# Kernel tuning notes

Measured on AMD Instinct MI355X. Metric: run time of the kernel, lower is better.

Reference implementation:

```python
import jax, jax.numpy as jnp
import numpy as np

HOMO_BOOST_THRD = 0.5
HOMO_LOSS_WEIGHT = 100.0
EPS = 1e-8  # F.cosine_similarity default eps

N_NODES = 50000
N_EDGES = 1600000
D_FEAT = 128
N_TARGET = 5000
N_BKD = 500


def setup_inputs() -> dict:
    key = jax.random.key(0)
    k1, k2, k3, k4, k5 = jax.random.split(key, 5)
    edge_index = jax.random.randint(k1, (2, N_EDGES), 0, N_NODES, dtype=jnp.int64 if jax.config.jax_enable_x64 else jnp.int32)
    edge_weights = jax.random.uniform(k2, (N_EDGES,), dtype=jnp.float32)
    x = jax.random.normal(k3, (N_NODES, D_FEAT), dtype=jnp.float32)
    target_nodes = jax.random.randint(k4, (N_TARGET,), 0, N_NODES)
    bkd_nodes = jax.random.randint(k5, (N_BKD,), 0, N_NODES)
    return {"edge_index": edge_index, "edge_weights": edge_weights, "x": x,
            "target_nodes": target_nodes, "bkd_nodes": bkd_nodes}


def reference(edge_index, edge_weights, x, target_nodes, bkd_nodes):
    n = x.shape[0]
    # membership bitmaps replace per-edge python `in set` checks
    is_bkd = jnp.zeros((n,), dtype=bool).at[bkd_nodes].set(True)
    is_tgt = jnp.zeros((n,), dtype=bool).at[target_nodes].set(True)

    u, v = edge_index[0], edge_index[1]
    # dense_to_sparse in the original drops zero-weight edges
    mask = ((is_bkd[u] & is_tgt[v]) | (is_bkd[v] & is_tgt[u])) & (edge_weights != 0)

    xu = x[u]  # [E, d]
    xv = x[v]  # [E, d]
    dot = jnp.sum(xu * xv, axis=-1)
    nu = jnp.maximum(jnp.linalg.norm(xu, axis=-1), EPS)
    nv = jnp.maximum(jnp.linalg.norm(xv, axis=-1), EPS)
    sims = dot / (nu * nv)  # F.cosine_similarity

    per_edge = jnp.maximum(HOMO_BOOST_THRD - sims, 0.0)  # clamp-at-zero branch
    loss = HOMO_LOSS_WEIGHT * jnp.sum(jnp.where(mask, per_edge, 0.0))
    return loss
```

## Files before the change

### kernel.cpp

```cpp
#include <hip/hip_runtime.h>

#define HOMO_BOOST_THRD 0.5f
#define HOMO_LOSS_WEIGHT 100.0f
#define COS_EPS 1e-8f
#define D_FEAT 128
#define EDGE_BLOCK 256
#define EPT 8
#define QMAX (EDGE_BLOCK * EPT)

#define FLAG_WORDS_MAX 4096

__global__ __launch_bounds__(EDGE_BLOCK) void edge_loss_kernel(
        const int* __restrict__ edge_index,
        const float* __restrict__ edge_weights,
        const float* __restrict__ x,
        const int* __restrict__ target_nodes, int n_tgt,
        const int* __restrict__ bkd_nodes, int n_bkd,
        float* __restrict__ partials, int E, int nwords) {
    __shared__ unsigned int sflags[FLAG_WORDS_MAX];
    __shared__ int q_u[QMAX];
    __shared__ int q_v[QMAX];
    __shared__ int qn;
    __shared__ float wsum[EDGE_BLOCK / 64];

    uint4* s4 = reinterpret_cast<uint4*>(sflags);
    const int nwords4 = (nwords + 3) >> 2;
    for (int i = threadIdx.x; i < nwords4; i += EDGE_BLOCK)
        s4[i] = make_uint4(0u, 0u, 0u, 0u);
    if (threadIdx.x == 0) qn = 0;
    __syncthreads();

    const int n_tgt4 = n_tgt >> 2;
    const int4* t4 = reinterpret_cast<const int4*>(target_nodes);
    for (int i = threadIdx.x; i < n_tgt4; i += EDGE_BLOCK) {
        int4 nd = t4[i];
        atomicOr(&sflags[nd.x >> 4], 2u << ((nd.x & 15) * 2));
        atomicOr(&sflags[nd.y >> 4], 2u << ((nd.y & 15) * 2));
        atomicOr(&sflags[nd.z >> 4], 2u << ((nd.z & 15) * 2));
        atomicOr(&sflags[nd.w >> 4], 2u << ((nd.w & 15) * 2));
    }
    for (int i = (n_tgt4 << 2) + threadIdx.x; i < n_tgt; i += EDGE_BLOCK) {
        int node = target_nodes[i];
        atomicOr(&sflags[node >> 4], 2u << ((node & 15) * 2));
    }
    const int n_bkd4 = n_bkd >> 2;
    const int4* b4 = reinterpret_cast<const int4*>(bkd_nodes);
    for (int i = threadIdx.x; i < n_bkd4; i += EDGE_BLOCK) {
        int4 nd = b4[i];
        atomicOr(&sflags[nd.x >> 4], 1u << ((nd.x & 15) * 2));
        atomicOr(&sflags[nd.y >> 4], 1u << ((nd.y & 15) * 2));
        atomicOr(&sflags[nd.z >> 4], 1u << ((nd.z & 15) * 2));
        atomicOr(&sflags[nd.w >> 4], 1u << ((nd.w & 15) * 2));
    }
    for (int i = (n_bkd4 << 2) + threadIdx.x; i < n_bkd; i += EDGE_BLOCK) {
        int node = bkd_nodes[i];
        atomicOr(&sflags[node >> 4], 1u << ((node & 15) * 2));
    }
    __syncthreads();

    const int base = (blockIdx.x * EDGE_BLOCK + threadIdx.x) * EPT;
    const bool full = (blockIdx.x * EDGE_BLOCK * EPT + EDGE_BLOCK * EPT <= E)
                      && ((E & 3) == 0);

    int us[EPT], vs[EPT];
    if (full) {
        const int4* up = reinterpret_cast<const int4*>(edge_index + base);
        const int4* vp = reinterpret_cast<const int4*>(edge_index + E + base);
        #pragma unroll
        for (int qd = 0; qd < EPT / 4; ++qd) {
            int4 uq = up[qd];
            int4 vq = vp[qd];
            us[qd*4+0] = uq.x; us[qd*4+1] = uq.y; us[qd*4+2] = uq.z; us[qd*4+3] = uq.w;
            vs[qd*4+0] = vq.x; vs[qd*4+1] = vq.y; vs[qd*4+2] = vq.z; vs[qd*4+3] = vq.w;
        }
    } else {
        #pragma unroll
        for (int k = 0; k < EPT; ++k) {
            int e = base + k;
            bool ok = (e < E);
            us[k] = ok ? edge_index[e] : 0;
            vs[k] = ok ? edge_index[E + e] : 0;
        }
    }

    #pragma unroll
    for (int k = 0; k < EPT; ++k) {
        bool valid = full || (base + k < E);
        unsigned fu = (sflags[us[k] >> 4] >> ((us[k] & 15) * 2)) & 3u;
        unsigned fv = (sflags[vs[k] >> 4] >> ((vs[k] & 15) * 2)) & 3u;
        bool m = valid && ((((fu & (fv >> 1)) | (fv & (fu >> 1))) & 1u) != 0);
        if (m) {
            float w = edge_weights[base + k];
            if (w != 0.0f) {
                int qi = atomicAdd(&qn, 1);
                q_u[qi] = us[k];
                q_v[qi] = vs[k];
            }
        }
    }
    __syncthreads();

    const int lane = threadIdx.x & 63;
    const int wid  = threadIdx.x >> 6;
    const int nq   = qn;
    float wval = 0.0f;

    for (int i = wid * 2; i < nq; i += 2 * (EDGE_BLOCK / 64)) {
        bool has1 = (i + 1 < nq);
        int u0 = q_u[i], v0 = q_v[i];
        int u1 = has1 ? q_u[i + 1] : u0;
        int v1 = has1 ? q_v[i + 1] : v0;

        float2 a0 = reinterpret_cast<const float2*>(x + (size_t)u0 * D_FEAT)[lane];
        float2 c0 = reinterpret_cast<const float2*>(x + (size_t)v0 * D_FEAT)[lane];
        float2 a1 = reinterpret_cast<const float2*>(x + (size_t)u1 * D_FEAT)[lane];
        float2 c1 = reinterpret_cast<const float2*>(x + (size_t)v1 * D_FEAT)[lane];

        float d0 = a0.x * c0.x + a0.y * c0.y;
        float p0 = a0.x * a0.x + a0.y * a0.y;
        float q0 = c0.x * c0.x + c0.y * c0.y;
        float d1 = a1.x * c1.x + a1.y * c1.y;
        float p1 = a1.x * a1.x + a1.y * a1.y;
        float q1 = c1.x * c1.x + c1.y * c1.y;
        #pragma unroll
        for (int off = 1; off < 64; off <<= 1) {
            d0 += __shfl_xor(d0, off, 64);
            p0 += __shfl_xor(p0, off, 64);
            q0 += __shfl_xor(q0, off, 64);
            d1 += __shfl_xor(d1, off, 64);
            p1 += __shfl_xor(p1, off, 64);
            q1 += __shfl_xor(q1, off, 64);
        }
        if (lane == 0) {
            float nu0 = fmaxf(sqrtf(p0), COS_EPS);
            float nv0 = fmaxf(sqrtf(q0), COS_EPS);
            wval += fmaxf(HOMO_BOOST_THRD - d0 / (nu0 * nv0), 0.0f);
            if (has1) {
                float nu1 = fmaxf(sqrtf(p1), COS_EPS);
                float nv1 = fmaxf(sqrtf(q1), COS_EPS);
                wval += fmaxf(HOMO_BOOST_THRD - d1 / (nu1 * nv1), 0.0f);
            }
        }
    }

    if (lane == 0) wsum[wid] = wval;
    __syncthreads();
    if (threadIdx.x == 0)
        partials[blockIdx.x] = wsum[0] + wsum[1] + wsum[2] + wsum[3];
}

__global__ void reduce_kernel(const float* __restrict__ partials, int n,
                              float* __restrict__ out) {
    __shared__ float wsum[16];
    float s = 0.0f;
    for (int i = threadIdx.x; i < n; i += blockDim.x) s += partials[i];
    #pragma unroll
    for (int off = 32; off > 0; off >>= 1) s += __shfl_down(s, off, 64);
    if ((threadIdx.x & 63) == 0) wsum[threadIdx.x >> 6] = s;
    __syncthreads();
    if (threadIdx.x == 0) {
        float t = 0.0f;
        for (int w = 0; w < (int)(blockDim.x >> 6); ++w) t += wsum[w];
        out[0] = t * HOMO_LOSS_WEIGHT;
    }
}

extern "C" void kernel_launch(void* const* d_in, const int* in_sizes, int n_in,
                              void* d_out, int out_size, void* d_ws, size_t ws_size,
                              hipStream_t stream) {
    const int*   edge_index   = (const int*)  d_in[0];
    const float* edge_weights = (const float*)d_in[1];
    const float* x            = (const float*)d_in[2];
    const int*   target_nodes = (const int*)  d_in[3];
    const int*   bkd_nodes    = (const int*)  d_in[4];

    const int E     = in_sizes[0] / 2;
    const int N     = in_sizes[2] / D_FEAT;
    const int n_tgt = in_sizes[3];
    const int n_bkd = in_sizes[4];

    const int nwords = (N + 15) / 16;
    float* partials = (float*)d_ws;

    const int nblocks = (E + EDGE_BLOCK * EPT - 1) / (EDGE_BLOCK * EPT);
    edge_loss_kernel<<<nblocks, EDGE_BLOCK, 0, stream>>>(
        edge_index, edge_weights, x, target_nodes, n_tgt, bkd_nodes, n_bkd,
        partials, E, nwords);

    reduce_kernel<<<1, 1024, 0, stream>>>(partials, nblocks, (float*)d_out);
}
```

Measured before the change: 13.58 us.

## Build membership bitmap once in a separate kernel and copy into shared memory

Moves construction of the backdoor/target bitmap out of every edge block into a single one-block prekernel that writes it to workspace. Each edge block then copies the prebuilt bitmap into shared memory instead of zeroing it and running about 5500 shared atomics. The block size also doubles to 512, which halves the number of blocks, and the final reduce uses 512 threads. The cost is an extra kernel launch that runs serially before the main kernel, plus a global read of the bitmap in every block.

```diff
diff --git a/kernel.cpp b/kernel.cpp
--- a/kernel.cpp
+++ b/kernel.cpp
@@ -4,63 +4,71 @@
 #define HOMO_LOSS_WEIGHT 100.0f
 #define COS_EPS 1e-8f
 #define D_FEAT 128
-#define EDGE_BLOCK 256
+#define EDGE_BLOCK 512
 #define EPT 8
+#define NWAVES (EDGE_BLOCK / 64)
 #define QMAX (EDGE_BLOCK * EPT)
 
 #define FLAG_WORDS_MAX 4096
+
+__global__ void build_flags_kernel(const int* __restrict__ target_nodes, int n_tgt,
+                                   const int* __restrict__ bkd_nodes, int n_bkd,
+                                   unsigned int* __restrict__ flags_w, int nwords) {
+    uint4* f4 = reinterpret_cast<uint4*>(flags_w);
+    const int nwords4 = (nwords + 3) >> 2;
+    for (int i = threadIdx.x; i < nwords4; i += blockDim.x)
+        f4[i] = make_uint4(0u, 0u, 0u, 0u);
+    __syncthreads();
+
+    const int n_tgt4 = n_tgt >> 2;
+    const int4* t4 = reinterpret_cast<const int4*>(target_nodes);
+    for (int i = threadIdx.x; i < n_tgt4; i += blockDim.x) {
+        int4 nd = t4[i];
+        atomicOr(&flags_w[nd.x >> 4], 2u << ((nd.x & 15) * 2));
+        atomicOr(&flags_w[nd.y >> 4], 2u << ((nd.y & 15) * 2));
+        atomicOr(&flags_w[nd.z >> 4], 2u << ((nd.z & 15) * 2));
+        atomicOr(&flags_w[nd.w >> 4], 2u << ((nd.w & 15) * 2));
+    }
+    for (int i = (n_tgt4 << 2) + threadIdx.x; i < n_tgt; i += blockDim.x) {
+        int node = target_nodes[i];
+        atomicOr(&flags_w[node >> 4], 2u << ((node & 15) * 2));
+    }
+    const int n_bkd4 = n_bkd >> 2;
+    const int4* b4 = reinterpret_cast<const int4*>(bkd_nodes);
+    for (int i = threadIdx.x; i < n_bkd4; i += blockDim.x) {
+        int4 nd = b4[i];
+        atomicOr(&flags_w[nd.x >> 4], 1u << ((nd.x & 15) * 2));
+        atomicOr(&flags_w[nd.y >> 4], 1u << ((nd.y & 15) * 2));
+        atomicOr(&flags_w[nd.z >> 4], 1u << ((nd.z & 15) * 2));
+        atomicOr(&flags_w[nd.w >> 4], 1u << ((nd.w & 15) * 2));
+    }
+    for (int i = (n_bkd4 << 2) + threadIdx.x; i < n_bkd; i += blockDim.x) {
+        int node = bkd_nodes[i];
+        atomicOr(&flags_w[node >> 4], 1u << ((node & 15) * 2));
+    }
+}
 
 __global__ __launch_bounds__(EDGE_BLOCK) void edge_loss_kernel(
         const int* __restrict__ edge_index,
         const float* __restrict__ edge_weights,
         const float* __restrict__ x,
-        const int* __restrict__ target_nodes, int n_tgt,
-        const int* __restrict__ bkd_nodes, int n_bkd,
+        const unsigned int* __restrict__ flags_w,
         float* __restrict__ partials, int E, int nwords) {
     __shared__ unsigned int sflags[FLAG_WORDS_MAX];
     __shared__ int q_u[QMAX];
     __shared__ int q_v[QMAX];
     __shared__ int qn;
-    __shared__ float wsum[EDGE_BLOCK / 64];
+    __shared__ float wsum[NWAVES];
 
     uint4* s4 = reinterpret_cast<uint4*>(sflags);
+    const uint4* f4 = reinterpret_cast<const uint4*>(flags_w);
     const int nwords4 = (nwords + 3) >> 2;
-    for (int i = threadIdx.x; i < nwords4; i += EDGE_BLOCK)
-        s4[i] = make_uint4(0u, 0u, 0u, 0u);
+    for (int i = threadIdx.x; i < nwords4; i += EDGE_BLOCK) s4[i] = f4[i];
     if (threadIdx.x == 0) qn = 0;
     __syncthreads();
 
-    const int n_tgt4 = n_tgt >> 2;
-    const int4* t4 = reinterpret_cast<const int4*>(target_nodes);
-    for (int i = threadIdx.x; i < n_tgt4; i += EDGE_BLOCK) {
-        int4 nd = t4[i];
-        atomicOr(&sflags[nd.x >> 4], 2u << ((nd.x & 15) * 2));
-        atomicOr(&sflags[nd.y >> 4], 2u << ((nd.y & 15) * 2));
-        atomicOr(&sflags[nd.z >> 4], 2u << ((nd.z & 15) * 2));
-        atomicOr(&sflags[nd.w >> 4], 2u << ((nd.w & 15) * 2));
-    }
-    for (int i = (n_tgt4 << 2) + threadIdx.x; i < n_tgt; i += EDGE_BLOCK) {
-        int node = target_nodes[i];
-        atomicOr(&sflags[node >> 4], 2u << ((node & 15) * 2));
-    }
-    const int n_bkd4 = n_bkd >> 2;
-    const int4* b4 = reinterpret_cast<const int4*>(bkd_nodes);
-    for (int i = threadIdx.x; i < n_bkd4; i += EDGE_BLOCK) {
-        int4 nd = b4[i];
-        atomicOr(&sflags[nd.x >> 4], 1u << ((nd.x & 15) * 2));
-        atomicOr(&sflags[nd.y >> 4], 1u << ((nd.y & 15) * 2));
-        atomicOr(&sflags[nd.z >> 4], 1u << ((nd.z & 15) * 2));
-        atomicOr(&sflags[nd.w >> 4], 1u << ((nd.w & 15) * 2));
-    }
-    for (int i = (n_bkd4 << 2) + threadIdx.x; i < n_bkd; i += EDGE_BLOCK) {
-        int node = bkd_nodes[i];
-        atomicOr(&sflags[node >> 4], 1u << ((node & 15) * 2));
-    }
-    __syncthreads();
-
     const int base = (blockIdx.x * EDGE_BLOCK + threadIdx.x) * EPT;
-    const bool full = (blockIdx.x * EDGE_BLOCK * EPT + EDGE_BLOCK * EPT <= E)
-                      && ((E & 3) == 0);
+    const bool full = ((blockIdx.x + 1) * EDGE_BLOCK * EPT <= E) && ((E & 3) == 0);
 
     int us[EPT], vs[EPT];
     if (full) {
@@ -105,7 +113,7 @@
     const int nq   = qn;
     float wval = 0.0f;
 
-    for (int i = wid * 2; i < nq; i += 2 * (EDGE_BLOCK / 64)) {
+    for (int i = wid * 2; i < nq; i += 2 * NWAVES) {
         bool has1 = (i + 1 < nq);
         int u0 = q_u[i], v0 = q_v[i];
         int u1 = has1 ? q_u[i + 1] : u0;
@@ -145,13 +153,17 @@
 
     if (lane == 0) wsum[wid] = wval;
     __syncthreads();
-    if (threadIdx.x == 0)
-        partials[blockIdx.x] = wsum[0] + wsum[1] + wsum[2] + wsum[3];
+    if (threadIdx.x == 0) {
+        float b = 0.0f;
+        #pragma unroll
+        for (int w = 0; w < NWAVES; ++w) b += wsum[w];
+        partials[blockIdx.x] = b;
+    }
 }
 
 __global__ void reduce_kernel(const float* __restrict__ partials, int n,
                               float* __restrict__ out) {
-    __shared__ float wsum[16];
+    __shared__ float wsum[8];
     float s = 0.0f;
     for (int i = threadIdx.x; i < n; i += blockDim.x) s += partials[i];
     #pragma unroll
@@ -180,12 +192,15 @@
     const int n_bkd = in_sizes[4];
 
     const int nwords = (N + 15) / 16;
-    float* partials = (float*)d_ws;
+    unsigned int* flags_w = (unsigned int*)d_ws;
+    float* partials = (float*)((char*)d_ws + 16384);
+
+    build_flags_kernel<<<1, 1024, 0, stream>>>(
+        target_nodes, n_tgt, bkd_nodes, n_bkd, flags_w, nwords);
 
     const int nblocks = (E + EDGE_BLOCK * EPT - 1) / (EDGE_BLOCK * EPT);
     edge_loss_kernel<<<nblocks, EDGE_BLOCK, 0, stream>>>(
-        edge_index, edge_weights, x, target_nodes, n_tgt, bkd_nodes, n_bkd,
-        partials, E, nwords);
-
-    reduce_kernel<<<1, 1024, 0, stream>>>(partials, nblocks, (float*)d_out);
-}
+        edge_index, edge_weights, x, flags_w, partials, E, nwords);
+
+    reduce_kernel<<<1, 512, 0, stream>>>(partials, nblocks, (float*)d_out);
+}
```

Result: slower. 22.52 us (+65.9%).

## Enlarge edge blocks to 1024 threads with bounded queue and overflow fallback

Applied to the files above, without the earlier changes.

Raises the block size from 256 to 1024 threads, so each block covers four times as many edges and the per-block bitmap build from target and backdoor nodes is repeated four times less often. The shared-memory queue is capped at 1024 packed int2 entries. Edges that overflow it are handled immediately by wave-cooperative inline computation. The final reduce now launches 256 threads over the smaller set of partials. The trade-off is fewer blocks (about 196) on a GPU with many CUs, plus possible divergence in the overflow path.

```diff
diff --git a/kernel.cpp b/kernel.cpp
--- a/kernel.cpp
+++ b/kernel.cpp
@@ -4,9 +4,10 @@
 #define HOMO_LOSS_WEIGHT 100.0f
 #define COS_EPS 1e-8f
 #define D_FEAT 128
-#define EDGE_BLOCK 256
+#define EDGE_BLOCK 1024
 #define EPT 8
-#define QMAX (EDGE_BLOCK * EPT)
+#define NWAVES (EDGE_BLOCK / 64)
+#define QMAX 1024
 
 #define FLAG_WORDS_MAX 4096
 
@@ -18,10 +19,9 @@
         const int* __restrict__ bkd_nodes, int n_bkd,
         float* __restrict__ partials, int E, int nwords) {
     __shared__ unsigned int sflags[FLAG_WORDS_MAX];
-    __shared__ int q_u[QMAX];
-    __shared__ int q_v[QMAX];
+    __shared__ int2 q[QMAX];
     __shared__ int qn;
-    __shared__ float wsum[EDGE_BLOCK / 64];
+    __shared__ float wsum[NWAVES];
 
     uint4* s4 = reinterpret_cast<uint4*>(sflags);
     const int nwords4 = (nwords + 3) >> 2;
@@ -58,9 +58,9 @@
     }
     __syncthreads();
 
+    const int lane = threadIdx.x & 63;
     const int base = (blockIdx.x * EDGE_BLOCK + threadIdx.x) * EPT;
-    const bool full = (blockIdx.x * EDGE_BLOCK * EPT + EDGE_BLOCK * EPT <= E)
-                      && ((E & 3) == 0);
+    const bool full = ((blockIdx.x + 1) * EDGE_BLOCK * EPT <= E) && ((E & 3) == 0);
 
     int us[EPT], vs[EPT];
     if (full) {
@@ -82,6 +82,8 @@
             vs[k] = ok ? edge_index[E + e] : 0;
         }
     }
+
+    float wval = 0.0f;
 
     #pragma unroll
     for (int k = 0; k < EPT; ++k) {
@@ -89,32 +91,53 @@
         unsigned fu = (sflags[us[k] >> 4] >> ((us[k] & 15) * 2)) & 3u;
         unsigned fv = (sflags[vs[k] >> 4] >> ((vs[k] & 15) * 2)) & 3u;
         bool m = valid && ((((fu & (fv >> 1)) | (fv & (fu >> 1))) & 1u) != 0);
+        bool ovf = false;
         if (m) {
             float w = edge_weights[base + k];
             if (w != 0.0f) {
                 int qi = atomicAdd(&qn, 1);
-                q_u[qi] = us[k];
-                q_v[qi] = vs[k];
-            }
-        }
-    }
-    __syncthreads();
-
-    const int lane = threadIdx.x & 63;
-    const int wid  = threadIdx.x >> 6;
-    const int nq   = qn;
-    float wval = 0.0f;
-
-    for (int i = wid * 2; i < nq; i += 2 * (EDGE_BLOCK / 64)) {
+                if (qi < QMAX) q[qi] = make_int2(us[k], vs[k]);
+                else ovf = true;
+            }
+        }
+        unsigned long long ob = __ballot(ovf);
+        while (ob) {
+            int b = __ffsll(ob) - 1;
+            ob &= ob - 1;
+            int eu = __shfl(us[k], b, 64);
+            int ev = __shfl(vs[k], b, 64);
+            float2 a = reinterpret_cast<const float2*>(x + (size_t)eu * D_FEAT)[lane];
+            float2 c = reinterpret_cast<const float2*>(x + (size_t)ev * D_FEAT)[lane];
+            float d = a.x * c.x + a.y * c.y;
+            float p = a.x * a.x + a.y * a.y;
+            float qq = c.x * c.x + c.y * c.y;
+            #pragma unroll
+            for (int off = 1; off < 64; off <<= 1) {
+                d += __shfl_xor(d, off, 64);
+                p += __shfl_xor(p, off, 64);
+                qq += __shfl_xor(qq, off, 64);
+            }
+            if (lane == 0) {
+                float nu = fmaxf(sqrtf(p), COS_EPS);
+                float nv = fmaxf(sqrtf(qq), COS_EPS);
+                wval += fmaxf(HOMO_BOOST_THRD - d / (nu * nv), 0.0f);
+            }
+        }
+    }
+    __syncthreads();
+
+    const int wid = threadIdx.x >> 6;
+    const int nq  = (qn < QMAX) ? qn : QMAX;
+
+    for (int i = wid * 2; i < nq; i += 2 * NWAVES) {
         bool has1 = (i + 1 < nq);
-        int u0 = q_u[i], v0 = q_v[i];
-        int u1 = has1 ? q_u[i + 1] : u0;
-        int v1 = has1 ? q_v[i + 1] : v0;
-
-        float2 a0 = reinterpret_cast<const float2*>(x + (size_t)u0 * D_FEAT)[lane];
-        float2 c0 = reinterpret_cast<const float2*>(x + (size_t)v0 * D_FEAT)[lane];
-        float2 a1 = reinterpret_cast<const float2*>(x + (size_t)u1 * D_FEAT)[lane];
-        float2 c1 = reinterpret_cast<const float2*>(x + (size_t)v1 * D_FEAT)[lane];
+        int2 e0 = q[i];
+        int2 e1 = has1 ? q[i + 1] : e0;
+
+        float2 a0 = reinterpret_cast<const float2*>(x + (size_t)e0.x * D_FEAT)[lane];
+        float2 c0 = reinterpret_cast<const float2*>(x + (size_t)e0.y * D_FEAT)[lane];
+        float2 a1 = reinterpret_cast<const float2*>(x + (size_t)e1.x * D_FEAT)[lane];
+        float2 c1 = reinterpret_cast<const float2*>(x + (size_t)e1.y * D_FEAT)[lane];
 
         float d0 = a0.x * c0.x + a0.y * c0.y;
         float p0 = a0.x * a0.x + a0.y * a0.y;
@@ -145,13 +168,17 @@
 
     if (lane == 0) wsum[wid] = wval;
     __syncthreads();
-    if (threadIdx.x == 0)
-        partials[blockIdx.x] = wsum[0] + wsum[1] + wsum[2] + wsum[3];
+    if (threadIdx.x == 0) {
+        float bsum = 0.0f;
+        #pragma unroll
+        for (int w = 0; w < NWAVES; ++w) bsum += wsum[w];
+        partials[blockIdx.x] = bsum;
+    }
 }
 
 __global__ void reduce_kernel(const float* __restrict__ partials, int n,
                               float* __restrict__ out) {
-    __shared__ float wsum[16];
+    __shared__ float wsum[4];
     float s = 0.0f;
     for (int i = threadIdx.x; i < n; i += blockDim.x) s += partials[i];
     #pragma unroll
@@ -187,5 +214,5 @@
         edge_index, edge_weights, x, target_nodes, n_tgt, bkd_nodes, n_bkd,
         partials, E, nwords);
 
-    reduce_kernel<<<1, 1024, 0, stream>>>(partials, nblocks, (float*)d_out);
+    reduce_kernel<<<1, 256, 0, stream>>>(partials, nblocks, (float*)d_out);
 }
```

Result: slower. 14.10 us (+3.8%).
